# Kernel optimization log

Measured on AMD Instinct MI355X. Metric: run time of the kernel, lower is better.

The kernel has to match this reference:

```python
import jax, jax.numpy as jnp
import numpy as np

N = 50000
E = 800000
D_IN = 128
D_OUT = 128


def setup_inputs() -> dict:
    key = jax.random.key(0)
    k1, k2, k3 = jax.random.split(key, 3)
    seq = jax.random.normal(k1, (N, D_IN), dtype=jnp.float32)
    edge_index = jax.random.randint(k2, (2, E), 0, N, dtype=jnp.int32)
    # Glorot-ish init for the GCNConv linear weight [in, out]
    W = jax.random.normal(k3, (D_IN, D_OUT), dtype=jnp.float32) * (1.0 / np.sqrt(D_IN))
    b = jnp.zeros((D_OUT,), dtype=jnp.float32)
    prelu_w = jnp.full((1,), 0.25, dtype=jnp.float32)
    return {"seq": seq, "edge_index": edge_index, "W": W, "b": b, "prelu_w": prelu_w}


def reference(seq, edge_index, W, b, prelu_w):
    # GCNConv: linear transform, add self-loops, symmetric normalization,
    # scatter-add aggregation, bias; then PReLU activation.
    n = seq.shape[0]
    xW = seq @ W  # [N, D_OUT]

    # add self-loops
    loop = jnp.arange(n, dtype=edge_index.dtype)
    row = jnp.concatenate([edge_index[0], loop])  # source
    col = jnp.concatenate([edge_index[1], loop])  # target

    # degree of target nodes (edge weight = 1)
    deg = jax.ops.segment_sum(jnp.ones_like(col, dtype=xW.dtype), col, num_segments=n)
    dinv = jnp.where(deg > 0, jax.lax.rsqrt(deg), 0.0)
    norm = dinv[row] * dinv[col]  # [E+N]

    msg = xW[row] * norm[:, None]  # gather + scale
    out = jax.ops.segment_sum(msg, col, num_segments=n)  # scatter-add
    out = out + b

    # PReLU with single shared weight
    return jnp.where(out > 0, out, prelu_w[0] * out)
```

## Files before the change

### kernel.cpp

```cpp
#include <hip/hip_runtime.h>

constexpr int D = 128;
constexpr int CAP = 64;
constexpr int OVFCAP = 65536;

__device__ __forceinline__ unsigned short f2bf(float f) {
    unsigned u = __float_as_uint(f);
    u += 0x7fffu + ((u >> 16) & 1u);
    return (unsigned short)(u >> 16);
}

__global__ __launch_bounds__(256) void k_place_gemm(
        const int* __restrict__ row, const int* __restrict__ col,
        int* __restrict__ deg, int* __restrict__ slots,
        int* __restrict__ ovfCnt, int2* __restrict__ ovf, int E,
        int gemmBlocks,
        const float* __restrict__ seq, const float* __restrict__ W,
        unsigned short* __restrict__ y16, int n) {
    __shared__ float sS[64 * D];
    __shared__ float sW[16 * D];

    int b = (int)blockIdx.x;
    int half = b >> 1;
    bool isGemm = ((b & 1) == 0) && (half < gemmBlocks);

    if (!isGemm) {
        int pIdx = (b < 2 * gemmBlocks) ? half : (b - gemmBlocks);
        int t = pIdx * 256 + threadIdx.x;
        int e = 2 * t;
        if (e + 1 < E) {
            int2 c2 = *(const int2*)(col + e);
            int2 r2 = *(const int2*)(row + e);
            int p0 = atomicAdd(&deg[c2.x], 1);
            int p1 = atomicAdd(&deg[c2.y], 1);
            if (p0 < CAP) slots[(size_t)c2.x * CAP + p0] = r2.x;
            else { int o = atomicAdd(ovfCnt, 1); if (o < OVFCAP) ovf[o] = make_int2(r2.x, c2.x); }
            if (p1 < CAP) slots[(size_t)c2.y * CAP + p1] = r2.y;
            else { int o = atomicAdd(ovfCnt, 1); if (o < OVFCAP) ovf[o] = make_int2(r2.y, c2.y); }
        } else if (e < E) {
            int c = col[e];
            int r = row[e];
            int p = atomicAdd(&deg[c], 1);
            if (p < CAP) slots[(size_t)c * CAP + p] = r;
            else { int o = atomicAdd(ovfCnt, 1); if (o < OVFCAP) ovf[o] = make_int2(r, c); }
        }
        return;
    }

    int row0 = half * 64;
    int rows = n - row0; if (rows > 64) rows = 64;

    {
        const float4* src = (const float4*)(seq + (size_t)row0 * D);
        float4* dst = (float4*)sS;
        int nf4 = rows * (D / 4);
        for (int i = threadIdx.x; i < nf4; i += 256) dst[i] = src[i];
    }

    int cg = threadIdx.x & 31;
    int rg = threadIdx.x >> 5;
    float4 acc[8];
    #pragma unroll
    for (int j = 0; j < 8; ++j) acc[j] = make_float4(0.f, 0.f, 0.f, 0.f);

    for (int kc = 0; kc < 8; ++kc) {
        __syncthreads();
        {
            const float4* wsrc = (const float4*)(W + (size_t)kc * 16 * D);
            float4* wdst = (float4*)sW;
            wdst[threadIdx.x]       = wsrc[threadIdx.x];
            wdst[threadIdx.x + 256] = wsrc[threadIdx.x + 256];
        }
        __syncthreads();
        int kbase = kc * 16;
        #pragma unroll
        for (int k2 = 0; k2 < 16; ++k2) {
            float4 w = ((const float4*)sW)[k2 * 32 + cg];
            int k = kbase + k2;
            #pragma unroll
            for (int j = 0; j < 8; ++j) {
                float s = sS[(rg * 8 + j) * D + k];
                acc[j].x = fmaf(s, w.x, acc[j].x);
                acc[j].y = fmaf(s, w.y, acc[j].y);
                acc[j].z = fmaf(s, w.z, acc[j].z);
                acc[j].w = fmaf(s, w.w, acc[j].w);
            }
        }
    }

    #pragma unroll
    for (int j = 0; j < 8; ++j) {
        int g = row0 + rg * 8 + j;
        if (g < n) {
            ushort4 o;
            o.x = f2bf(acc[j].x);
            o.y = f2bf(acc[j].y);
            o.z = f2bf(acc[j].z);
            o.w = f2bf(acc[j].w);
            *(ushort4*)(y16 + (size_t)g * D + cg * 4) = o;
        }
    }
}

__global__ __launch_bounds__(256) void k_agg(
        const int* __restrict__ slots, const int* __restrict__ deg,
        const int* __restrict__ ovfCnt, const int2* __restrict__ ovf,
        const unsigned short* __restrict__ y16,
        const float* __restrict__ b, const float* __restrict__ pw,
        float* __restrict__ out, int n) {
    int wid = (blockIdx.x * 256 + threadIdx.x) >> 6;
    if (wid >= n) return;
    int lane = threadIdx.x & 63;

    int cntf = deg[wid];
    int cnt = cntf < CAP ? cntf : CAP;
    float dc = rsqrtf((float)(cntf + 1));

    unsigned sv = *(const unsigned*)(y16 + (size_t)wid * D + 2 * lane);
    float ax0 = __uint_as_float(sv << 16) * dc;
    float ay0 = __uint_as_float(sv & 0xffff0000u) * dc;
    float ax1 = 0.f, ay1 = 0.f, ax2 = 0.f, ay2 = 0.f, ax3 = 0.f, ay3 = 0.f;
    float ax4 = 0.f, ay4 = 0.f, ax5 = 0.f, ay5 = 0.f, ax6 = 0.f, ay6 = 0.f;
    float ax7 = 0.f, ay7 = 0.f;

    int my = (lane < cnt) ? slots[(size_t)wid * CAP + lane] : 0;

    int k = 0;
    for (; k + 7 < cnt; k += 8) {
        int r0 = __shfl(my, k);
        int r1 = __shfl(my, k + 1);
        int r2 = __shfl(my, k + 2);
        int r3 = __shfl(my, k + 3);
        int r4 = __shfl(my, k + 4);
        int r5 = __shfl(my, k + 5);
        int r6 = __shfl(my, k + 6);
        int r7 = __shfl(my, k + 7);
        int g0 = deg[r0]; int g1 = deg[r1]; int g2 = deg[r2]; int g3 = deg[r3];
        int g4 = deg[r4]; int g5 = deg[r5]; int g6 = deg[r6]; int g7 = deg[r7];
        unsigned v0 = *(const unsigned*)(y16 + (size_t)r0 * D + 2 * lane);
        unsigned v1 = *(const unsigned*)(y16 + (size_t)r1 * D + 2 * lane);
        unsigned v2 = *(const unsigned*)(y16 + (size_t)r2 * D + 2 * lane);
        unsigned v3 = *(const unsigned*)(y16 + (size_t)r3 * D + 2 * lane);
        unsigned v4 = *(const unsigned*)(y16 + (size_t)r4 * D + 2 * lane);
        unsigned v5 = *(const unsigned*)(y16 + (size_t)r5 * D + 2 * lane);
        unsigned v6 = *(const unsigned*)(y16 + (size_t)r6 * D + 2 * lane);
        unsigned v7 = *(const unsigned*)(y16 + (size_t)r7 * D + 2 * lane);
        float dr0 = rsqrtf((float)(g0 + 1));
        float dr1 = rsqrtf((float)(g1 + 1));
        float dr2 = rsqrtf((float)(g2 + 1));
        float dr3 = rsqrtf((float)(g3 + 1));
        float dr4 = rsqrtf((float)(g4 + 1));
        float dr5 = rsqrtf((float)(g5 + 1));
        float dr6 = rsqrtf((float)(g6 + 1));
        float dr7 = rsqrtf((float)(g7 + 1));
        ax0 = fmaf(__uint_as_float(v0 << 16), dr0, ax0); ay0 = fmaf(__uint_as_float(v0 & 0xffff0000u), dr0, ay0);
        ax1 = fmaf(__uint_as_float(v1 << 16), dr1, ax1); ay1 = fmaf(__uint_as_float(v1 & 0xffff0000u), dr1, ay1);
        ax2 = fmaf(__uint_as_float(v2 << 16), dr2, ax2); ay2 = fmaf(__uint_as_float(v2 & 0xffff0000u), dr2, ay2);
        ax3 = fmaf(__uint_as_float(v3 << 16), dr3, ax3); ay3 = fmaf(__uint_as_float(v3 & 0xffff0000u), dr3, ay3);
        ax4 = fmaf(__uint_as_float(v4 << 16), dr4, ax4); ay4 = fmaf(__uint_as_float(v4 & 0xffff0000u), dr4, ay4);
        ax5 = fmaf(__uint_as_float(v5 << 16), dr5, ax5); ay5 = fmaf(__uint_as_float(v5 & 0xffff0000u), dr5, ay5);
        ax6 = fmaf(__uint_as_float(v6 << 16), dr6, ax6); ay6 = fmaf(__uint_as_float(v6 & 0xffff0000u), dr6, ay6);
        ax7 = fmaf(__uint_as_float(v7 << 16), dr7, ax7); ay7 = fmaf(__uint_as_float(v7 & 0xffff0000u), dr7, ay7);
    }
    for (; k < cnt; ++k) {
        int r = __shfl(my, k);
        float dr = rsqrtf((float)(deg[r] + 1));
        unsigned v = *(const unsigned*)(y16 + (size_t)r * D + 2 * lane);
        ax0 = fmaf(__uint_as_float(v << 16), dr, ax0);
        ay0 = fmaf(__uint_as_float(v & 0xffff0000u), dr, ay0);
    }

    if (cntf > CAP) {
        int m = *ovfCnt; if (m > OVFCAP) m = OVFCAP;
        for (int j = 0; j < m; ++j) {
            int2 pr = ovf[j];
            if (pr.y == wid) {
                float dr = rsqrtf((float)(deg[pr.x] + 1));
                unsigned v = *(const unsigned*)(y16 + (size_t)pr.x * D + 2 * lane);
                ax0 = fmaf(__uint_as_float(v << 16), dr, ax0);
                ay0 = fmaf(__uint_as_float(v & 0xffff0000u), dr, ay0);
            }
        }
    }

    float sx = ((ax0 + ax1) + (ax2 + ax3)) + ((ax4 + ax5) + (ax6 + ax7));
    float sy = ((ay0 + ay1) + (ay2 + ay3)) + ((ay4 + ay5) + (ay6 + ay7));

    float2 bb = *(const float2*)(b + 2 * lane);
    float p = pw[0];
    float vx = sx * dc + bb.x;
    float vy = sy * dc + bb.y;
    vx = vx > 0.f ? vx : p * vx;
    vy = vy > 0.f ? vy : p * vy;
    *(float2*)(out + (size_t)wid * D + 2 * lane) = make_float2(vx, vy);
}

extern "C" void kernel_launch(void* const* d_in, const int* in_sizes, int n_in,
                              void* d_out, int out_size, void* d_ws, size_t ws_size,
                              hipStream_t stream) {
    const float* seq = (const float*)d_in[0];
    const int*   ei  = (const int*)d_in[1];
    const float* W   = (const float*)d_in[2];
    const float* b   = (const float*)d_in[3];
    const float* pw  = (const float*)d_in[4];
    int n = in_sizes[0] / D;
    int E = in_sizes[1] / 2;

    float* out = (float*)d_out;

    auto align = [](size_t x) { return (x + 255) & ~(size_t)255; };
    char* p = (char*)d_ws;
    unsigned short* y16 = (unsigned short*)p; p += align((size_t)n * D * sizeof(unsigned short));
    int*  deg    = (int*)p;   size_t degBytes = align((size_t)n * sizeof(int)); p += degBytes;
    int*  ovfCnt = (int*)p;   p += 256;
    int2* ovf    = (int2*)p;  p += align((size_t)OVFCAP * sizeof(int2));
    int*  slots  = (int*)p;   p += align((size_t)n * CAP * sizeof(int));

    hipMemsetAsync(deg, 0, degBytes + 256, stream);

    int GB = (n + 63) / 64;
    int PB = (E + 511) / 512;
    k_place_gemm<<<GB + PB, 256, 0, stream>>>(
        ei, ei + E, deg, slots, ovfCnt, ovf, E, GB, seq, W, y16, n);

    k_agg<<<(unsigned)(((long long)n * 64 + 255) / 256), 256, 0, stream>>>(
        slots, deg, ovfCnt, ovf, y16, b, pw, out, n);
}
```

Before: 100.3 us.

## Use bf16 MFMA for the dense transform with a pre-swizzled weight

Replaces the FP32 shared-memory FMA GEMM with MFMA 16x16x32 bf16 instructions. Each wave converts its seq rows to bf16 in registers, and a new prep kernel converts W to bf16 in the B-operand fragment layout so that lanes load it directly. This removes the shared-memory staging and the syncthreads, freeing LDS for occupancy. In exchange there is an extra small kernel launch, the inputs are quantized to bf16 before the multiply, and the output stores are 2-byte scattered writes.

```diff
diff --git a/kernel.cpp b/kernel.cpp
--- a/kernel.cpp
+++ b/kernel.cpp
@@ -3,11 +3,26 @@
 constexpr int D = 128;
 constexpr int CAP = 64;
 constexpr int OVFCAP = 65536;
+
+typedef __attribute__((ext_vector_type(8))) short short8;
+typedef __attribute__((ext_vector_type(4))) float f32x4;
 
 __device__ __forceinline__ unsigned short f2bf(float f) {
     unsigned u = __float_as_uint(f);
     u += 0x7fffu + ((u >> 16) & 1u);
     return (unsigned short)(u >> 16);
+}
+
+__global__ __launch_bounds__(256) void k_prep(const float* __restrict__ W,
+                                              unsigned short* __restrict__ Wf) {
+    int tid = blockIdx.x * 256 + threadIdx.x;
+    int j  = tid & 7;
+    int l  = (tid >> 3) & 63;
+    int g  = tid >> 9;
+    int kc = g >> 3, t = g & 7;
+    int k  = kc * 32 + ((l >> 4) * 4) + (j & 3) + ((j >> 2) * 16);
+    int c  = t * 16 + (l & 15);
+    Wf[tid] = f2bf(W[k * D + c]);
 }
 
 __global__ __launch_bounds__(256) void k_place_gemm(
@@ -15,11 +30,8 @@
         int* __restrict__ deg, int* __restrict__ slots,
         int* __restrict__ ovfCnt, int2* __restrict__ ovf, int E,
         int gemmBlocks,
-        const float* __restrict__ seq, const float* __restrict__ W,
+        const float* __restrict__ seq, const unsigned short* __restrict__ Wf,
         unsigned short* __restrict__ y16, int n) {
-    __shared__ float sS[64 * D];
-    __shared__ float sW[16 * D];
-
     int b = (int)blockIdx.x;
     int half = b >> 1;
     bool isGemm = ((b & 1) == 0) && (half < gemmBlocks);
@@ -47,57 +59,46 @@
         return;
     }
 
+    int w  = threadIdx.x >> 6;
+    int l  = threadIdx.x & 63;
+    int lr = l & 15;
+    int lg = l >> 4;
+
     int row0 = half * 64;
-    int rows = n - row0; if (rows > 64) rows = 64;
-
-    {
-        const float4* src = (const float4*)(seq + (size_t)row0 * D);
-        float4* dst = (float4*)sS;
-        int nf4 = rows * (D / 4);
-        for (int i = threadIdx.x; i < nf4; i += 256) dst[i] = src[i];
-    }
-
-    int cg = threadIdx.x & 31;
-    int rg = threadIdx.x >> 5;
-    float4 acc[8];
+    int m = row0 + w * 16 + lr;
+    if (m >= n) m = n - 1;
+    const float* sp = seq + (size_t)m * D;
+
+    f32x4 acc[8];
     #pragma unroll
-    for (int j = 0; j < 8; ++j) acc[j] = make_float4(0.f, 0.f, 0.f, 0.f);
-
-    for (int kc = 0; kc < 8; ++kc) {
-        __syncthreads();
-        {
-            const float4* wsrc = (const float4*)(W + (size_t)kc * 16 * D);
-            float4* wdst = (float4*)sW;
-            wdst[threadIdx.x]       = wsrc[threadIdx.x];
-            wdst[threadIdx.x + 256] = wsrc[threadIdx.x + 256];
-        }
-        __syncthreads();
-        int kbase = kc * 16;
+    for (int t = 0; t < 8; ++t) acc[t] = (f32x4){0.f, 0.f, 0.f, 0.f};
+
+    const short8* WfB = (const short8*)Wf;
+
+    #pragma unroll
+    for (int kc = 0; kc < 4; ++kc) {
+        int kb = kc * 32 + lg * 4;
+        float4 lo = *(const float4*)(sp + kb);
+        float4 hi = *(const float4*)(sp + kb + 16);
+        short8 a;
+        a[0] = (short)f2bf(lo.x); a[1] = (short)f2bf(lo.y);
+        a[2] = (short)f2bf(lo.z); a[3] = (short)f2bf(lo.w);
+        a[4] = (short)f2bf(hi.x); a[5] = (short)f2bf(hi.y);
+        a[6] = (short)f2bf(hi.z); a[7] = (short)f2bf(hi.w);
         #pragma unroll
-        for (int k2 = 0; k2 < 16; ++k2) {
-            float4 w = ((const float4*)sW)[k2 * 32 + cg];
-            int k = kbase + k2;
+        for (int t = 0; t < 8; ++t) {
+            short8 bf = WfB[(kc * 8 + t) * 64 + l];
+            acc[t] = __builtin_amdgcn_mfma_f32_16x16x32_bf16(a, bf, acc[t], 0, 0, 0);
+        }
+    }
+
+    #pragma unroll
+    for (int i = 0; i < 4; ++i) {
+        int g = row0 + w * 16 + lg * 4 + i;
+        if (g < n) {
+            unsigned short* yp = y16 + (size_t)g * D + lr;
             #pragma unroll
-            for (int j = 0; j < 8; ++j) {
-                float s = sS[(rg * 8 + j) * D + k];
-                acc[j].x = fmaf(s, w.x, acc[j].x);
-                acc[j].y = fmaf(s, w.y, acc[j].y);
-                acc[j].z = fmaf(s, w.z, acc[j].z);
-                acc[j].w = fmaf(s, w.w, acc[j].w);
-            }
-        }
-    }
-
-    #pragma unroll
-    for (int j = 0; j < 8; ++j) {
-        int g = row0 + rg * 8 + j;
-        if (g < n) {
-            ushort4 o;
-            o.x = f2bf(acc[j].x);
-            o.y = f2bf(acc[j].y);
-            o.z = f2bf(acc[j].z);
-            o.w = f2bf(acc[j].w);
-            *(ushort4*)(y16 + (size_t)g * D + cg * 4) = o;
+            for (int t = 0; t < 8; ++t) yp[t * 16] = f2bf(acc[t][i]);
         }
     }
 }
@@ -215,13 +216,15 @@
     int*  ovfCnt = (int*)p;   p += 256;
     int2* ovf    = (int2*)p;  p += align((size_t)OVFCAP * sizeof(int2));
     int*  slots  = (int*)p;   p += align((size_t)n * CAP * sizeof(int));
+    unsigned short* Wf = (unsigned short*)p; p += align((size_t)D * D * sizeof(unsigned short));
 
     hipMemsetAsync(deg, 0, degBytes + 256, stream);
+    k_prep<<<64, 256, 0, stream>>>(W, Wf);
 
     int GB = (n + 63) / 64;
     int PB = (E + 511) / 512;
     k_place_gemm<<<GB + PB, 256, 0, stream>>>(
-        ei, ei + E, deg, slots, ovfCnt, ovf, E, GB, seq, W, y16, n);
+        ei, ei + E, deg, slots, ovfCnt, ovf, E, GB, seq, Wf, y16, n);
 
     k_agg<<<(unsigned)(((long long)n * 64 + 255) / 256), 256, 0, stream>>>(
         slots, deg, ovfCnt, ovf, y16, b, pw, out, n);
```

Measured after the change: 99.37 us. Within noise of the previous version (-1.0%).
